# Kernel tuning notes

Hardware: AMD Instinct MI355X
Metric: run time of the kernel (lower is better)

Reference implementation:

```python
import jax, jax.numpy as jnp
import numpy as np

N_NODES = 50000
N_EDGES = 800000
IN_C, OUT_C, EDGE_F, HEADS, HID, FINAL = 8, 16, 8, 4, 64, 128
NEG_SLOPE = 0.2  # PyG GATConv default LeakyReLU slope


def setup_inputs() -> dict:
    key = jax.random.key(0)
    ks = jax.random.split(key, 12)
    s = 0.1
    return {
        "x": jax.random.normal(ks[0], (N_NODES, IN_C), jnp.float32),
        "edge_index": jax.random.randint(ks[1], (2, N_EDGES), 0, N_NODES, jnp.int64),
        "edge_attr": jax.random.normal(ks[2], (N_EDGES, EDGE_F), jnp.float32),
        # NNConv params: root weight, bias, edge-MLP Linear(EDGE_F -> IN_C*OUT_C)
        "ecc_root": jax.random.normal(ks[3], (IN_C, OUT_C), jnp.float32) * s,
        "ecc_bias": jnp.zeros((OUT_C,), jnp.float32),
        "mlp_w": jax.random.normal(ks[4], (EDGE_F, IN_C * OUT_C), jnp.float32) * s,
        "mlp_b": jnp.zeros((IN_C * OUT_C,), jnp.float32),
        # GATConv params
        "gat_lin": jax.random.normal(ks[5], (OUT_C, HEADS * HID), jnp.float32) * s,
        "att_src": jax.random.normal(ks[6], (HEADS, HID), jnp.float32) * s,
        "att_dst": jax.random.normal(ks[7], (HEADS, HID), jnp.float32) * s,
        "gat_bias": jnp.zeros((HEADS * HID,), jnp.float32),
        # final Linear
        "fc_w": jax.random.normal(ks[8], (HEADS * HID, FINAL), jnp.float32) * s,
        "fc_b": jnp.zeros((FINAL,), jnp.float32),
    }


def _forward(x, edge_index, edge_attr, ecc_root, ecc_bias, mlp_w, mlp_b,
             gat_lin, att_src, att_dst, gat_bias, fc_w, fc_b):
    src, dst = edge_index[0], edge_index[1]  # messages flow src -> dst

    # ---- NNConv (edge-conditioned conv), aggr='add' ----
    # per-edge weight matrices [E, IN_C, OUT_C] from edge MLP
    w_e = (edge_attr @ mlp_w + mlp_b).reshape(-1, IN_C, OUT_C)
    msg = jnp.einsum('ei,eio->eo', x[src], w_e)                 # [E, OUT_C]
    agg = jax.ops.segment_sum(msg, dst, num_segments=N_NODES)   # [N, OUT_C]
    h = jax.nn.relu(x @ ecc_root + agg + ecc_bias)              # [N, OUT_C]

    # ---- GATConv (heads concatenated) ----
    g = (h @ gat_lin).reshape(N_NODES, HEADS, HID)              # [N, H, D]
    a_src = jnp.einsum('nhd,hd->nh', g, att_src)                # [N, H]
    a_dst = jnp.einsum('nhd,hd->nh', g, att_dst)
    e = jax.nn.leaky_relu(a_src[src] + a_dst[dst], NEG_SLOPE)   # [E, H]
    # segment softmax over incoming edges of each dst node
    e_max = jax.ops.segment_max(e, dst, num_segments=N_NODES)   # [N, H]
    e_max = jnp.where(jnp.isfinite(e_max), e_max, 0.0)
    e_exp = jnp.exp(e - e_max[dst])                             # [E, H]
    denom = jax.ops.segment_sum(e_exp, dst, num_segments=N_NODES)
    alpha = e_exp / (denom[dst] + 1e-16)                        # [E, H]
    out = jax.ops.segment_sum(alpha[:, :, None] * g[src], dst,
                              num_segments=N_NODES)             # [N, H, D]
    out = jax.nn.relu(out.reshape(N_NODES, HEADS * HID) + gat_bias)

    # ---- final linear ----
    return out @ fc_w + fc_b                                    # [N, FINAL]


def reference(x, edge_index, edge_attr, ecc_root, ecc_bias, mlp_w, mlp_b,
              gat_lin, att_src, att_dst, gat_bias, fc_w, fc_b):
    return _forward(x, edge_index, edge_attr, ecc_root, ecc_bias, mlp_w, mlp_b,
                    gat_lin, att_src, att_dst, gat_bias, fc_w, fc_b)
```

## Files before the change

### kernel.cpp

```cpp
#include <hip/hip_runtime.h>

#define N_NODES 50000
#define N_EDGES 800000
#define IN_C 8
#define OUT_C 16
#define EDGE_F 8
#define HEADS 4
#define HID 64
#define GDIM (HEADS*HID)
#define FINAL 128
#define NEG_SLOPE 0.2f
#define EB ((N_EDGES+255)/256)
#define NBLK 196

__device__ __forceinline__ int clampn(int v) {
    return v < 0 ? 0 : (v >= N_NODES ? N_NODES - 1 : v);
}
__device__ __forceinline__ unsigned short f32_to_bf16(float f) {
    unsigned u = __float_as_uint(f);
    unsigned r = (u + 0x7fffu + ((u >> 16) & 1u)) >> 16;
    return (unsigned short)r;
}
__device__ __forceinline__ float bf16lo(unsigned u) { return __uint_as_float(u << 16); }
__device__ __forceinline__ float bf16hi(unsigned u) { return __uint_as_float(u & 0xffff0000u); }

__global__ __launch_bounds__(256) void k_hist(const int* __restrict__ dst,
                                              int* __restrict__ cnt,
                                              int* __restrict__ rnk)
{
    int e = blockIdx.x * 256 + threadIdx.x;
    if (e >= N_EDGES) return;
    rnk[e] = atomicAdd(&cnt[clampn(dst[e])], 1);
}

__global__ __launch_bounds__(256) void k_part(const int* __restrict__ cnt,
                                              int* __restrict__ part)
{
    int i = blockIdx.x * 256 + threadIdx.x;
    int v = (i < N_NODES) ? cnt[i] : 0;
#pragma unroll
    for (int off = 32; off; off >>= 1) v += __shfl_down(v, off);
    __shared__ int ws[4];
    if ((threadIdx.x & 63) == 0) ws[threadIdx.x >> 6] = v;
    __syncthreads();
    if (threadIdx.x == 0) part[blockIdx.x] = ws[0] + ws[1] + ws[2] + ws[3];
}

__global__ __launch_bounds__(256) void k_scan1(const int* __restrict__ part,
                                               int* __restrict__ partscan)
{
    int t = threadIdx.x;
    int v = (t < NBLK) ? part[t] : 0;
    int lane = t & 63, wid = t >> 6;
    int incl = v;
#pragma unroll
    for (int off = 1; off < 64; off <<= 1) {
        int u = __shfl_up(incl, off);
        if (lane >= off) incl += u;
    }
    __shared__ int wsum[4];
    if (lane == 63) wsum[wid] = incl;
    __syncthreads();
    int add = 0;
    for (int w = 0; w < wid; w++) add += wsum[w];
    partscan[t] = incl - v + add;
}

__global__ __launch_bounds__(256) void k_add(const int* __restrict__ cnt,
                                             const int* __restrict__ partscan,
                                             int* __restrict__ offs)
{
    int i = blockIdx.x * 256 + threadIdx.x;
    int v = (i < N_NODES) ? cnt[i] : 0;
    int lane = threadIdx.x & 63, wid = threadIdx.x >> 6;
    int incl = v;
#pragma unroll
    for (int off = 1; off < 64; off <<= 1) {
        int u = __shfl_up(incl, off);
        if (lane >= off) incl += u;
    }
    __shared__ int wsum[4];
    if (lane == 63) wsum[wid] = incl;
    __syncthreads();
    int add = partscan[blockIdx.x];
    for (int w = 0; w < wid; w++) add += wsum[w];
    if (i < N_NODES) offs[i] = incl - v + add;
    if (i == 0) offs[N_NODES] = N_EDGES;
}

__global__ __launch_bounds__(256) void k_scatter(
    const int* __restrict__ src, const int* __restrict__ dst,
    const int* __restrict__ rnk, const int* __restrict__ offs,
    int2* __restrict__ se_csr)
{
    int e = blockIdx.x * 256 + threadIdx.x;
    if (e >= N_EDGES) return;
    int p = offs[clampn(dst[e])] + rnk[e];
    se_csr[p] = make_int2(clampn(src[e]), e);
}

__global__ __launch_bounds__(256) void k2T_node(
    const float* __restrict__ x,
    const int2* __restrict__ se_csr, const int* __restrict__ offs,
    const float* __restrict__ ea,
    const float* __restrict__ mlp_w, const float* __restrict__ mlp_b,
    const float* __restrict__ ecc_root, const float* __restrict__ ecc_bias,
    const float* __restrict__ gat_lin,
    const float* __restrict__ att_src_w, const float* __restrict__ att_dst_w,
    unsigned short* __restrict__ g_bf, float* __restrict__ asrc, float* __restrict__ adst)
{
    __shared__ float smW[EDGE_F * IN_C * OUT_C];
    __shared__ float smb[IN_C * OUT_C];
    __shared__ float sT[4][64];
    __shared__ float sxs[4][8];
    for (int i = threadIdx.x; i < EDGE_F * IN_C * OUT_C; i += 256) smW[i] = mlp_w[i];
    for (int i = threadIdx.x; i < IN_C * OUT_C; i += 256) smb[i] = mlp_b[i];

    int wid = threadIdx.x >> 6, lane = threadIdx.x & 63;
    int n = blockIdx.x * 4 + wid;
    bool alive = (n < N_NODES);

    float t0 = 0.f, t1 = 0.f, t2 = 0.f, t3 = 0.f, xs = 0.f;
    if (alive) {
        int f = lane >> 3, i = lane & 7;
        int beg = offs[n], end = offs[n + 1];
        int j = beg;
        for (; j + 3 < end; j += 4) {
            int2 se0 = se_csr[j],     se1 = se_csr[j + 1];
            int2 se2 = se_csr[j + 2], se3 = se_csr[j + 3];
            float a0 = ea[(size_t)se0.y * EDGE_F + f];
            float a1 = ea[(size_t)se1.y * EDGE_F + f];
            float a2 = ea[(size_t)se2.y * EDGE_F + f];
            float a3 = ea[(size_t)se3.y * EDGE_F + f];
            float x0 = x[se0.x * IN_C + i];
            float x1 = x[se1.x * IN_C + i];
            float x2 = x[se2.x * IN_C + i];
            float x3 = x[se3.x * IN_C + i];
            t0 += a0 * x0; t1 += a1 * x1; t2 += a2 * x2; t3 += a3 * x3;
            xs += (x0 + x1) + (x2 + x3);
        }
        for (; j < end; j++) {
            int2 se = se_csr[j];
            float a = ea[(size_t)se.y * EDGE_F + f];
            float xv = x[se.x * IN_C + i];
            t0 += a * xv;
            xs += xv;
        }
        sT[wid][lane] = (t0 + t1) + (t2 + t3);
        if (f == 0) sxs[wid][i] = xs;
    }
    __syncthreads();
    if (!alive) return;

    int o = lane & 15;
    float hv = 0.f;
    if (lane < 16) {
        float v = ecc_bias[o];
#pragma unroll 8
        for (int jj = 0; jj < 64; jj++)
            v += smW[jj * OUT_C + o] * sT[wid][jj];
#pragma unroll
        for (int ii = 0; ii < IN_C; ii++) {
            v += smb[ii * OUT_C + o] * sxs[wid][ii];
            v += x[n * IN_C + ii] * ecc_root[ii * OUT_C + o];
        }
        hv = fmaxf(v, 0.f);
    }

    float gv[4] = {0.f, 0.f, 0.f, 0.f};
#pragma unroll
    for (int k = 0; k < OUT_C; k++) {
        float hk = __shfl(hv, k);
#pragma unroll
        for (int j = 0; j < 4; j++)
            gv[j] += hk * gat_lin[k * GDIM + j * 64 + lane];
    }
#pragma unroll
    for (int j = 0; j < 4; j++)
        g_bf[(size_t)n * GDIM + j * 64 + lane] = f32_to_bf16(gv[j]);

    float vs[4], vd[4];
#pragma unroll
    for (int j = 0; j < 4; j++) {
        vs[j] = gv[j] * att_src_w[j * 64 + lane];
        vd[j] = gv[j] * att_dst_w[j * 64 + lane];
    }
#pragma unroll
    for (int off = 32; off; off >>= 1) {
#pragma unroll
        for (int j = 0; j < 4; j++) {
            vs[j] += __shfl_down(vs[j], off);
            vd[j] += __shfl_down(vd[j], off);
        }
    }
    if (lane == 0) {
#pragma unroll
        for (int j = 0; j < 4; j++) {
            asrc[n * HEADS + j] = vs[j];
            adst[n * HEADS + j] = vd[j];
        }
    }
}

__global__ __launch_bounds__(256) void k_gat(
    const int* __restrict__ offs, const int2* __restrict__ se_csr,
    const float* __restrict__ asrc, const float* __restrict__ adst,
    const unsigned short* __restrict__ g_bf, unsigned short* __restrict__ outg)
{
    int n = blockIdx.x, t = threadIdx.x;
    int lane32 = t & 31, grp = t >> 5;
    int hh = lane32 >> 3;
    int beg = offs[n], deg = offs[n + 1] - beg;

    float adsth = adst[n * HEADS + hh];

    float acc[8];
#pragma unroll
    for (int k = 0; k < 8; k++) acc[k] = 0.f;
    float denp = 0.f;

    for (int j = grp; j < deg; j += 8) {
        int s = se_csr[beg + j].x;
        float v = asrc[s * HEADS + hh] + adsth;
        v = v > 0.f ? v : NEG_SLOPE * v;
        float p = __expf(v);
        denp += p;
        uint4 gv = *(const uint4*)&g_bf[(size_t)s * GDIM + lane32 * 8];
        acc[0] += p * bf16lo(gv.x);
        acc[1] += p * bf16hi(gv.x);
        acc[2] += p * bf16lo(gv.y);
        acc[3] += p * bf16hi(gv.y);
        acc[4] += p * bf16lo(gv.z);
        acc[5] += p * bf16hi(gv.z);
        acc[6] += p * bf16lo(gv.w);
        acc[7] += p * bf16hi(gv.w);
    }

    __shared__ float s_acc[8][GDIM];
    __shared__ float s_den[8][HEADS];
    *(float4*)&s_acc[grp][lane32 * 8]     = make_float4(acc[0], acc[1], acc[2], acc[3]);
    *(float4*)&s_acc[grp][lane32 * 8 + 4] = make_float4(acc[4], acc[5], acc[6], acc[7]);
    if ((lane32 & 7) == 0) s_den[grp][hh] = denp;
    __syncthreads();

    int head = t >> 6;
    float den = 0.f, v = 0.f;
#pragma unroll
    for (int g2 = 0; g2 < 8; g2++) {
        den += s_den[g2][head];
        v += s_acc[g2][t];
    }
    outg[(size_t)n * GDIM + t] = f32_to_bf16(v / (den + 1e-16f));
}

#define BM 64
#define BK6 16
__global__ __launch_bounds__(256) void k6_final(
    const unsigned short* __restrict__ outg, const float* __restrict__ gat_bias,
    const float* __restrict__ fc_w, const float* __restrict__ fc_b,
    float* __restrict__ y)
{
    __shared__ float sA[BK6][BM + 4];
    __shared__ float sW[BK6][FINAL];
    int tid = threadIdx.x;
    int r0 = blockIdx.x * BM;
    int tcol = (tid & 31) * 4;
    int trow = (tid >> 5) * 8;

    float acc[8][4];
#pragma unroll
    for (int r = 0; r < 8; r++)
#pragma unroll
        for (int c = 0; c < 4; c++) acc[r][c] = 0.f;

    int ar = tid >> 2;
    int ak = (tid & 3) * 4;

    for (int k0 = 0; k0 < GDIM; k0 += BK6) {
        int row = r0 + ar;
        float4 av = make_float4(0.f, 0.f, 0.f, 0.f);
        if (row < N_NODES) {
            uint2 raw = *(const uint2*)&outg[(size_t)row * GDIM + k0 + ak];
            av = make_float4(bf16lo(raw.x), bf16hi(raw.x), bf16lo(raw.y), bf16hi(raw.y));
        }
        float4 bv = *(const float4*)&gat_bias[k0 + ak];
        av.x = fmaxf(av.x + bv.x, 0.f);
        av.y = fmaxf(av.y + bv.y, 0.f);
        av.z = fmaxf(av.z + bv.z, 0.f);
        av.w = fmaxf(av.w + bv.w, 0.f);
        sA[ak + 0][ar] = av.x;
        sA[ak + 1][ar] = av.y;
        sA[ak + 2][ar] = av.z;
        sA[ak + 3][ar] = av.w;
#pragma unroll
        for (int p = 0; p < 2; p++) {
            int kk = (tid >> 5) + p * 8;
            int c = (tid & 31) * 4;
            *(float4*)&sW[kk][c] = *(const float4*)&fc_w[(size_t)(k0 + kk) * FINAL + c];
        }
        __syncthreads();
#pragma unroll
        for (int kk = 0; kk < BK6; kk++) {
            float4 w = *(const float4*)&sW[kk][tcol];
            float4 a0 = *(const float4*)&sA[kk][trow];
            float4 a1 = *(const float4*)&sA[kk][trow + 4];
            float a[8] = {a0.x, a0.y, a0.z, a0.w, a1.x, a1.y, a1.z, a1.w};
#pragma unroll
            for (int r = 0; r < 8; r++) {
                acc[r][0] += a[r] * w.x;
                acc[r][1] += a[r] * w.y;
                acc[r][2] += a[r] * w.z;
                acc[r][3] += a[r] * w.w;
            }
        }
        __syncthreads();
    }

    float4 fb = *(const float4*)&fc_b[tcol];
#pragma unroll
    for (int r = 0; r < 8; r++) {
        int row = r0 + trow + r;
        if (row < N_NODES) {
            *(float4*)&y[(size_t)row * FINAL + tcol] =
                make_float4(acc[r][0] + fb.x, acc[r][1] + fb.y,
                            acc[r][2] + fb.z, acc[r][3] + fb.w);
        }
    }
}

extern "C" void kernel_launch(void* const* d_in, const int* in_sizes, int n_in,
                              void* d_out, int out_size, void* d_ws, size_t ws_size,
                              hipStream_t stream)
{
    const float* x        = (const float*)d_in[0];
    const int*   ei       = (const int*)d_in[1];
    const float* ea       = (const float*)d_in[2];
    const float* ecc_root = (const float*)d_in[3];
    const float* ecc_bias = (const float*)d_in[4];
    const float* mlp_w    = (const float*)d_in[5];
    const float* mlp_b    = (const float*)d_in[6];
    const float* gat_lin  = (const float*)d_in[7];
    const float* att_src  = (const float*)d_in[8];
    const float* att_dst  = (const float*)d_in[9];
    const float* gat_bias = (const float*)d_in[10];
    const float* fc_w     = (const float*)d_in[11];
    const float* fc_b     = (const float*)d_in[12];
    float* y = (float*)d_out;

    const int* src = ei;
    const int* dst = ei + N_EDGES;

    unsigned short* g_bf = (unsigned short*)d_ws;
    unsigned short* outg = g_bf + (size_t)N_NODES * GDIM;
    float* asrc = (float*)(outg + (size_t)N_NODES * GDIM);
    float* adst = asrc + (size_t)N_NODES * HEADS;
    int*   cnt      = (int*)(adst + (size_t)N_NODES * HEADS);
    int*   offs     = cnt + N_NODES;
    int*   part     = offs + N_NODES + 1;
    int*   partscan = part + 256;
    int*   rnk      = partscan + 256;
    int2*  se_csr   = (int2*)(rnk + N_EDGES);

    hipMemsetAsync(cnt, 0, sizeof(int) * N_NODES, stream);

    k_hist   <<<EB, 256, 0, stream>>>(dst, cnt, rnk);
    k_part   <<<NBLK, 256, 0, stream>>>(cnt, part);
    k_scan1  <<<1, 256, 0, stream>>>(part, partscan);
    k_add    <<<NBLK, 256, 0, stream>>>(cnt, partscan, offs);
    k_scatter<<<EB, 256, 0, stream>>>(src, dst, rnk, offs, se_csr);

    k2T_node <<<(N_NODES + 3) / 4, 256, 0, stream>>>(x, se_csr, offs, ea,
                                                     mlp_w, mlp_b,
                                                     ecc_root, ecc_bias, gat_lin,
                                                     att_src, att_dst, g_bf, asrc, adst);
    k_gat    <<<N_NODES, 256, 0, stream>>>(offs, se_csr, asrc, adst, g_bf, outg);
    k6_final <<<(N_NODES + BM - 1) / BM, 256, 0, stream>>>(outg, gat_bias, fc_w, fc_b, y);
}
```

Measured before the change: 374.3 us.

## Aggregate 16-dim hidden features in GAT and apply linear projection after aggregation

The attention logits are computed from h via precomposed weights, made by folding gat_lin with att_src/att_dst in a new small kernel. The GAT kernel gathers the 16-wide h per edge instead of the 256-wide bf16 g and applies gat_lin once per node after the softmax-weighted sum, cutting per-edge gather traffic sharply. The NNConv kernel now uses one block per node with four waves splitting the edge list, and the GAT kernel handles two nodes per block. In exchange, every GAT block reloads the 16x256 gat_lin into shared memory, and the per-node matvec adds some compute.

```diff
diff --git a/kernel.cpp b/kernel.cpp
--- a/kernel.cpp
+++ b/kernel.cpp
@@ -99,158 +99,162 @@
     se_csr[p] = make_int2(clampn(src[e]), e);
 }
 
-__global__ __launch_bounds__(256) void k2T_node(
+__global__ __launch_bounds__(64) void k_fold(
+    const float* __restrict__ gat_lin,
+    const float* __restrict__ att_src_w, const float* __restrict__ att_dst_w,
+    float* __restrict__ wsrc, float* __restrict__ wdst)
+{
+    int t = threadIdx.x;
+    int c = t >> 2, h = t & 3;
+    float ws = 0.f, wd = 0.f;
+    for (int k = 0; k < HID; k++) {
+        float l = gat_lin[c * GDIM + h * HID + k];
+        ws += l * att_src_w[h * HID + k];
+        wd += l * att_dst_w[h * HID + k];
+    }
+    wsrc[t] = ws;
+    wdst[t] = wd;
+}
+
+__global__ __launch_bounds__(256) void k2T_blk(
     const float* __restrict__ x,
     const int2* __restrict__ se_csr, const int* __restrict__ offs,
     const float* __restrict__ ea,
     const float* __restrict__ mlp_w, const float* __restrict__ mlp_b,
     const float* __restrict__ ecc_root, const float* __restrict__ ecc_bias,
-    const float* __restrict__ gat_lin,
-    const float* __restrict__ att_src_w, const float* __restrict__ att_dst_w,
-    unsigned short* __restrict__ g_bf, float* __restrict__ asrc, float* __restrict__ adst)
+    const float* __restrict__ wsrc, const float* __restrict__ wdst,
+    float* __restrict__ h_tab, float* __restrict__ asrc, float* __restrict__ adst)
 {
     __shared__ float smW[EDGE_F * IN_C * OUT_C];
     __shared__ float smb[IN_C * OUT_C];
+    __shared__ float sws[64], swd[64];
     __shared__ float sT[4][64];
     __shared__ float sxs[4][8];
+    __shared__ float sh[16];
     for (int i = threadIdx.x; i < EDGE_F * IN_C * OUT_C; i += 256) smW[i] = mlp_w[i];
-    for (int i = threadIdx.x; i < IN_C * OUT_C; i += 256) smb[i] = mlp_b[i];
-
-    int wid = threadIdx.x >> 6, lane = threadIdx.x & 63;
-    int n = blockIdx.x * 4 + wid;
-    bool alive = (n < N_NODES);
-
-    float t0 = 0.f, t1 = 0.f, t2 = 0.f, t3 = 0.f, xs = 0.f;
-    if (alive) {
-        int f = lane >> 3, i = lane & 7;
-        int beg = offs[n], end = offs[n + 1];
-        int j = beg;
-        for (; j + 3 < end; j += 4) {
-            int2 se0 = se_csr[j],     se1 = se_csr[j + 1];
-            int2 se2 = se_csr[j + 2], se3 = se_csr[j + 3];
-            float a0 = ea[(size_t)se0.y * EDGE_F + f];
-            float a1 = ea[(size_t)se1.y * EDGE_F + f];
-            float a2 = ea[(size_t)se2.y * EDGE_F + f];
-            float a3 = ea[(size_t)se3.y * EDGE_F + f];
-            float x0 = x[se0.x * IN_C + i];
-            float x1 = x[se1.x * IN_C + i];
-            float x2 = x[se2.x * IN_C + i];
-            float x3 = x[se3.x * IN_C + i];
-            t0 += a0 * x0; t1 += a1 * x1; t2 += a2 * x2; t3 += a3 * x3;
-            xs += (x0 + x1) + (x2 + x3);
-        }
-        for (; j < end; j++) {
-            int2 se = se_csr[j];
-            float a = ea[(size_t)se.y * EDGE_F + f];
-            float xv = x[se.x * IN_C + i];
-            t0 += a * xv;
-            xs += xv;
-        }
-        sT[wid][lane] = (t0 + t1) + (t2 + t3);
-        if (f == 0) sxs[wid][i] = xs;
-    }
-    __syncthreads();
-    if (!alive) return;
-
-    int o = lane & 15;
-    float hv = 0.f;
+    if (threadIdx.x < 128) smb[threadIdx.x] = mlp_b[threadIdx.x];
+    else if (threadIdx.x < 192) sws[threadIdx.x - 128] = wsrc[threadIdx.x - 128];
+    else swd[threadIdx.x - 192] = wdst[threadIdx.x - 192];
+
+    int w = threadIdx.x >> 6, lane = threadIdx.x & 63;
+    int n = blockIdx.x;
+    int f = lane >> 3, i = lane & 7;
+    int beg = offs[n], end = offs[n + 1];
+
+    float t0 = 0.f, t1 = 0.f, xs = 0.f;
+    int j = beg + w;
+    for (; j + 4 < end; j += 8) {
+        int2 se0 = se_csr[j], se1 = se_csr[j + 4];
+        float a0 = ea[(size_t)se0.y * EDGE_F + f];
+        float a1 = ea[(size_t)se1.y * EDGE_F + f];
+        float x0 = x[se0.x * IN_C + i];
+        float x1 = x[se1.x * IN_C + i];
+        t0 += a0 * x0; t1 += a1 * x1;
+        xs += x0 + x1;
+    }
+    for (; j < end; j += 4) {
+        int2 se = se_csr[j];
+        float a = ea[(size_t)se.y * EDGE_F + f];
+        float xv = x[se.x * IN_C + i];
+        t0 += a * xv;
+        xs += xv;
+    }
+    sT[w][lane] = t0 + t1;
+    if (f == 0) sxs[w][i] = xs;
+    __syncthreads();
+    if (w != 0) return;
+
+    float tf = sT[0][lane] + sT[1][lane] + sT[2][lane] + sT[3][lane];
+    sT[0][lane] = tf;
+    if (f == 0) sxs[0][i] = sxs[0][i] + sxs[1][i] + sxs[2][i] + sxs[3][i];
+
+    int o = lane;
     if (lane < 16) {
         float v = ecc_bias[o];
 #pragma unroll 8
         for (int jj = 0; jj < 64; jj++)
-            v += smW[jj * OUT_C + o] * sT[wid][jj];
+            v += smW[jj * OUT_C + o] * sT[0][jj];
 #pragma unroll
         for (int ii = 0; ii < IN_C; ii++) {
-            v += smb[ii * OUT_C + o] * sxs[wid][ii];
+            v += smb[ii * OUT_C + o] * sxs[0][ii];
             v += x[n * IN_C + ii] * ecc_root[ii * OUT_C + o];
         }
-        hv = fmaxf(v, 0.f);
-    }
-
-    float gv[4] = {0.f, 0.f, 0.f, 0.f};
-#pragma unroll
-    for (int k = 0; k < OUT_C; k++) {
-        float hk = __shfl(hv, k);
-#pragma unroll
-        for (int j = 0; j < 4; j++)
-            gv[j] += hk * gat_lin[k * GDIM + j * 64 + lane];
-    }
-#pragma unroll
-    for (int j = 0; j < 4; j++)
-        g_bf[(size_t)n * GDIM + j * 64 + lane] = f32_to_bf16(gv[j]);
-
-    float vs[4], vd[4];
-#pragma unroll
-    for (int j = 0; j < 4; j++) {
-        vs[j] = gv[j] * att_src_w[j * 64 + lane];
-        vd[j] = gv[j] * att_dst_w[j * 64 + lane];
-    }
-#pragma unroll
-    for (int off = 32; off; off >>= 1) {
-#pragma unroll
-        for (int j = 0; j < 4; j++) {
-            vs[j] += __shfl_down(vs[j], off);
-            vd[j] += __shfl_down(vd[j], off);
-        }
-    }
-    if (lane == 0) {
-#pragma unroll
-        for (int j = 0; j < 4; j++) {
-            asrc[n * HEADS + j] = vs[j];
-            adst[n * HEADS + j] = vd[j];
-        }
-    }
-}
-
-__global__ __launch_bounds__(256) void k_gat(
+        float hv = fmaxf(v, 0.f);
+        sh[o] = hv;
+        h_tab[n * OUT_C + o] = hv;
+    }
+    if (lane < 4) {
+        float as = 0.f, ad = 0.f;
+#pragma unroll
+        for (int c = 0; c < 16; c++) {
+            as += sh[c] * sws[c * 4 + lane];
+            ad += sh[c] * swd[c * 4 + lane];
+        }
+        asrc[n * HEADS + lane] = as;
+        adst[n * HEADS + lane] = ad;
+    }
+}
+
+__global__ __launch_bounds__(256) void k_gatU(
     const int* __restrict__ offs, const int2* __restrict__ se_csr,
     const float* __restrict__ asrc, const float* __restrict__ adst,
-    const unsigned short* __restrict__ g_bf, unsigned short* __restrict__ outg)
-{
-    int n = blockIdx.x, t = threadIdx.x;
-    int lane32 = t & 31, grp = t >> 5;
-    int hh = lane32 >> 3;
-    int beg = offs[n], deg = offs[n + 1] - beg;
-
-    float adsth = adst[n * HEADS + hh];
-
-    float acc[8];
-#pragma unroll
-    for (int k = 0; k < 8; k++) acc[k] = 0.f;
-    float denp = 0.f;
-
-    for (int j = grp; j < deg; j += 8) {
-        int s = se_csr[beg + j].x;
-        float v = asrc[s * HEADS + hh] + adsth;
-        v = v > 0.f ? v : NEG_SLOPE * v;
+    const float* __restrict__ h_tab, const float* __restrict__ gat_lin,
+    unsigned short* __restrict__ outg)
+{
+    __shared__ float slin[OUT_C * GDIM];
+    __shared__ float sU[4][64];
+    __shared__ float sden[4][HEADS];
+    for (int idx = threadIdx.x; idx < OUT_C * GDIM; idx += 256) slin[idx] = gat_lin[idx];
+
+    int t = threadIdx.x;
+    int w = t >> 6, lane = t & 63;
+    int local = w >> 1, q = w & 1;
+    int n = blockIdx.x * 2 + local;
+    int h = lane >> 4, c = lane & 15;
+    float adsth = adst[n * HEADS + h];
+    int beg = offs[n], end = offs[n + 1];
+
+    float U = 0.f, denp = 0.f;
+    int j = beg + q;
+    for (; j + 2 < end; j += 4) {
+        int2 se0 = se_csr[j], se1 = se_csr[j + 2];
+        float av0 = asrc[se0.x * HEADS + h];
+        float av1 = asrc[se1.x * HEADS + h];
+        float h0 = h_tab[se0.x * OUT_C + c];
+        float h1 = h_tab[se1.x * OUT_C + c];
+        float v0 = av0 + adsth; v0 = v0 > 0.f ? v0 : NEG_SLOPE * v0;
+        float v1 = av1 + adsth; v1 = v1 > 0.f ? v1 : NEG_SLOPE * v1;
+        float p0 = __expf(v0), p1 = __expf(v1);
+        denp += p0 + p1;
+        U += p0 * h0 + p1 * h1;
+    }
+    for (; j < end; j += 2) {
+        int2 se = se_csr[j];
+        float av = asrc[se.x * HEADS + h];
+        float hv = h_tab[se.x * OUT_C + c];
+        float v = av + adsth; v = v > 0.f ? v : NEG_SLOPE * v;
         float p = __expf(v);
         denp += p;
-        uint4 gv = *(const uint4*)&g_bf[(size_t)s * GDIM + lane32 * 8];
-        acc[0] += p * bf16lo(gv.x);
-        acc[1] += p * bf16hi(gv.x);
-        acc[2] += p * bf16lo(gv.y);
-        acc[3] += p * bf16hi(gv.y);
-        acc[4] += p * bf16lo(gv.z);
-        acc[5] += p * bf16hi(gv.z);
-        acc[6] += p * bf16lo(gv.w);
-        acc[7] += p * bf16hi(gv.w);
-    }
-
-    __shared__ float s_acc[8][GDIM];
-    __shared__ float s_den[8][HEADS];
-    *(float4*)&s_acc[grp][lane32 * 8]     = make_float4(acc[0], acc[1], acc[2], acc[3]);
-    *(float4*)&s_acc[grp][lane32 * 8 + 4] = make_float4(acc[4], acc[5], acc[6], acc[7]);
-    if ((lane32 & 7) == 0) s_den[grp][hh] = denp;
-    __syncthreads();
-
-    int head = t >> 6;
-    float den = 0.f, v = 0.f;
-#pragma unroll
-    for (int g2 = 0; g2 < 8; g2++) {
-        den += s_den[g2][head];
-        v += s_acc[g2][t];
-    }
-    outg[(size_t)n * GDIM + t] = f32_to_bf16(v / (den + 1e-16f));
+        U += p * hv;
+    }
+    sU[w][lane] = U;
+    if (c == 0) sden[w][h] = denp;
+    __syncthreads();
+    if (q != 0) return;
+
+    float U2 = sU[w][lane] + sU[w + 1][lane];
+    sU[w][lane] = U2;
+    if (c == 0) sden[w][h] = sden[w][h] + sden[w + 1][h];
+
+#pragma unroll
+    for (int j2 = 0; j2 < 4; j2++) {
+        float acc = 0.f;
+#pragma unroll
+        for (int cc = 0; cc < 16; cc++)
+            acc += sU[w][j2 * 16 + cc] * slin[cc * GDIM + j2 * 64 + lane];
+        float dv = sden[w][j2] + 1e-16f;
+        outg[(size_t)n * GDIM + j2 * 64 + lane] = f32_to_bf16(acc / dv);
+    }
 }
 
 #define BM 64
@@ -350,11 +354,13 @@
     const int* src = ei;
     const int* dst = ei + N_EDGES;
 
-    unsigned short* g_bf = (unsigned short*)d_ws;
-    unsigned short* outg = g_bf + (size_t)N_NODES * GDIM;
+    float* h_tab = (float*)d_ws;
+    unsigned short* outg = (unsigned short*)(h_tab + (size_t)N_NODES * OUT_C);
     float* asrc = (float*)(outg + (size_t)N_NODES * GDIM);
     float* adst = asrc + (size_t)N_NODES * HEADS;
-    int*   cnt      = (int*)(adst + (size_t)N_NODES * HEADS);
+    float* wsrc = adst + (size_t)N_NODES * HEADS;
+    float* wdst = wsrc + 64;
+    int*   cnt      = (int*)(wdst + 64);
     int*   offs     = cnt + N_NODES;
     int*   part     = offs + N_NODES + 1;
     int*   partscan = part + 256;
@@ -364,15 +370,16 @@
     hipMemsetAsync(cnt, 0, sizeof(int) * N_NODES, stream);
 
     k_hist   <<<EB, 256, 0, stream>>>(dst, cnt, rnk);
+    k_fold   <<<1, 64, 0, stream>>>(gat_lin, att_src, att_dst, wsrc, wdst);
     k_part   <<<NBLK, 256, 0, stream>>>(cnt, part);
     k_scan1  <<<1, 256, 0, stream>>>(part, partscan);
     k_add    <<<NBLK, 256, 0, stream>>>(cnt, partscan, offs);
     k_scatter<<<EB, 256, 0, stream>>>(src, dst, rnk, offs, se_csr);
 
-    k2T_node <<<(N_NODES + 3) / 4, 256, 0, stream>>>(x, se_csr, offs, ea,
-                                                     mlp_w, mlp_b,
-                                                     ecc_root, ecc_bias, gat_lin,
-                                                     att_src, att_dst, g_bf, asrc, adst);
-    k_gat    <<<N_NODES, 256, 0, stream>>>(offs, se_csr, asrc, adst, g_bf, outg);
+    k2T_blk  <<<N_NODES, 256, 0, stream>>>(x, se_csr, offs, ea, mlp_w, mlp_b,
+                                           ecc_root, ecc_bias, wsrc, wdst,
+                                           h_tab, asrc, adst);
+    k_gatU   <<<N_NODES / 2, 256, 0, stream>>>(offs, se_csr, asrc, adst,
+                                               h_tab, gat_lin, outg);
     k6_final <<<(N_NODES + BM - 1) / BM, 256, 0, stream>>>(outg, gat_bias, fc_w, fc_b, y);
 }
```

Result: slower. 415.6 us (+11.0%).
